# Performance work log

Measured on AMD Instinct MI355X. Metric: run time of the kernel, lower is better.

The kernel has to match this reference:

```python
import jax, jax.numpy as jnp
import numpy as np

D = 256; HEADS = 8; POINTS = 4; LAYERS = 6; HGT = 100; WID = 100; DH = D // HEADS


def _ln(x, g, b, eps=1e-5):
    m = x.mean(-1, keepdims=True)
    v = ((x - m) ** 2).mean(-1, keepdims=True)
    return (x - m) * jax.lax.rsqrt(v + eps) * g + b


def _bilinear(img, locs):
    # img: [B, H, W, C]; locs: [B, N, 2] normalized (x, y) in [0,1]
    # matches F.grid_sample(align_corners=False, padding_mode='zeros')
    B, H, W, C = img.shape
    flat = img.reshape(B, H * W, C)
    x = locs[..., 0] * W - 0.5
    y = locs[..., 1] * H - 0.5
    x0 = jnp.floor(x).astype(jnp.int32); y0 = jnp.floor(y).astype(jnp.int32)
    wx1 = x - x0; wx0 = 1.0 - wx1
    wy1 = y - y0; wy0 = 1.0 - wy1

    def corner(xi, yi, wgt):
        valid = (xi >= 0) & (xi < W) & (yi >= 0) & (yi < H)
        idx = jnp.clip(yi, 0, H - 1) * W + jnp.clip(xi, 0, W - 1)
        v = jnp.take_along_axis(flat, idx[..., None], axis=1)  # [B,N,C]
        return v * (wgt * valid)[..., None]

    return (corner(x0, y0, wx0 * wy0) + corner(x0 + 1, y0, wx1 * wy0)
            + corner(x0, y0 + 1, wx0 * wy1) + corner(x0 + 1, y0 + 1, wx1 * wy1))


def _forward(features, pos_embed, level_embed, off_w, off_b, aw_w, aw_b,
             val_w, val_b, out_w, out_b, ln1_g, ln1_b,
             ffn_w1, ffn_b1, ffn_w2, ffn_b2, ln3_g, ln3_b):
    bs, c, h, w = features.shape
    S = h * w
    src = features.reshape(bs, c, S).transpose(0, 2, 1)  # [bs,S,D]
    pos = pos_embed.reshape(bs, c, S).transpose(0, 2, 1) + level_embed[None, None, :]
    # reference points: pixel centers normalized; valid_ratios == 1 (no padding)
    ry = (jnp.arange(h, dtype=src.dtype) + 0.5) / h
    rx = (jnp.arange(w, dtype=src.dtype) + 0.5) / w
    ref = jnp.stack(jnp.meshgrid(rx, ry, indexing='xy'), -1).reshape(S, 2)  # [S,2] (x,y)
    norm = jnp.array([w, h], dtype=src.dtype)
    for l in range(LAYERS):
        q = src + pos  # with_pos_embed
        value = (src @ val_w[l] + val_b[l]).reshape(bs, S, HEADS, DH)
        off = (q @ off_w[l] + off_b[l]).reshape(bs, S, HEADS, POINTS, 2)
        attw = jax.nn.softmax((q @ aw_w[l] + aw_b[l]).reshape(bs, S, HEADS, POINTS), axis=-1)
        loc = ref[None, :, None, None, :] + off / norm  # [bs,S,H,P,2]
        img = value.transpose(0, 2, 1, 3).reshape(bs * HEADS, h, w, DH)
        locs = loc.transpose(0, 2, 1, 3, 4).reshape(bs * HEADS, S * POINTS, 2)
        samp = _bilinear(img, locs).reshape(bs, HEADS, S, POINTS, DH)
        attn = jnp.einsum('bhspd,bshp->bshd', samp, attw).reshape(bs, S, D)
        attn = attn @ out_w[l] + out_b[l]
        src = _ln(src + attn, ln1_g[l], ln1_b[l])  # norm1_xy (unit_dim*2 == d_model)
        ff = jax.nn.relu(src @ ffn_w1[l] + ffn_b1[l]) @ ffn_w2[l] + ffn_b2[l]
        src = _ln(src + ff, ln3_g[l], ln3_b[l])
    return src


def setup_inputs() -> dict:
    key = jax.random.key(0)
    ks = jax.random.split(key, 12)
    bs = 2
    s = 0.02
    rnd = lambda k, shape: jax.random.normal(k, shape, jnp.float32) * s
    return {
        'features': jax.random.normal(ks[0], (bs, D, HGT, WID), jnp.float32),
        'pos_embed': jax.random.normal(ks[1], (bs, D, HGT, WID), jnp.float32),
        'level_embed': rnd(ks[2], (D,)),
        'off_w': rnd(ks[3], (LAYERS, D, HEADS * POINTS * 2)),
        'off_b': rnd(ks[4], (LAYERS, HEADS * POINTS * 2)),
        'aw_w': rnd(ks[5], (LAYERS, D, HEADS * POINTS)),
        'aw_b': jnp.zeros((LAYERS, HEADS * POINTS), jnp.float32),
        'val_w': rnd(ks[6], (LAYERS, D, D)),
        'val_b': jnp.zeros((LAYERS, D), jnp.float32),
        'out_w': rnd(ks[7], (LAYERS, D, D)),
        'out_b': jnp.zeros((LAYERS, D), jnp.float32),
        'ln1_g': jnp.ones((LAYERS, D), jnp.float32),
        'ln1_b': jnp.zeros((LAYERS, D), jnp.float32),
        'ffn_w1': rnd(ks[8], (LAYERS, D, D)),
        'ffn_b1': jnp.zeros((LAYERS, D), jnp.float32),
        'ffn_w2': rnd(ks[9], (LAYERS, D, D)),
        'ffn_b2': jnp.zeros((LAYERS, D), jnp.float32),
        'ln3_g': jnp.ones((LAYERS, D), jnp.float32),
        'ln3_b': jnp.zeros((LAYERS, D), jnp.float32),
    }


def reference(features, pos_embed, level_embed, off_w, off_b, aw_w, aw_b,
              val_w, val_b, out_w, out_b, ln1_g, ln1_b,
              ffn_w1, ffn_b1, ffn_w2, ffn_b2, ln3_g, ln3_b):
    return _forward(features, pos_embed, level_embed, off_w, off_b, aw_w, aw_b,
                    val_w, val_b, out_w, out_b, ln1_g, ln1_b,
                    ffn_w1, ffn_b1, ffn_w2, ffn_b2, ln3_g, ln3_b)
```

## Files before the change

### kernel.cpp

```cpp
#include <hip/hip_runtime.h>
#include <math.h>

#define HGT 100
#define WID 100
#define S_TOK (HGT * WID)
#define D_MODEL 256
#define N_HEADS 8
#define DH 32
#define N_POINTS 4
#define N_LAYERS 6
#define BS 2
#define M_TOK (BS * S_TOK)

typedef __attribute__((ext_vector_type(8))) short short8v;
typedef __attribute__((ext_vector_type(4))) short short4v;
typedef __attribute__((ext_vector_type(4))) float f32x4;

__device__ __forceinline__ short f2bf(float f) {
  union { float f; unsigned u; } v; v.f = f;
  unsigned r = v.u + 0x7fff + ((v.u >> 16) & 1);
  return (short)(r >> 16);
}
__device__ __forceinline__ float bf2f(short s) {
  union { unsigned u; float f; } v;
  v.u = ((unsigned)(unsigned short)s) << 16;
  return v.f;
}

__global__ __launch_bounds__(256) void prep_tokens(
    const float* __restrict__ feat, const float* __restrict__ posin,
    const float* __restrict__ level, short* __restrict__ posb,
    short* __restrict__ srcb, short* __restrict__ qb) {
  __shared__ float tf[32][33];
  __shared__ float tp[32][33];
  int b = blockIdx.z;
  int s0 = blockIdx.x * 32;
  int c0 = blockIdx.y * 32;
  int tx = threadIdx.x, ty = threadIdx.y;
#pragma unroll
  for (int i = 0; i < 4; ++i) {
    int c = c0 + ty + i * 8;
    int s = s0 + tx;
    bool ok = s < S_TOK;
    size_t o = ((size_t)b * D_MODEL + c) * S_TOK + s;
    tf[ty + i * 8][tx] = ok ? feat[o] : 0.f;
    tp[ty + i * 8][tx] = ok ? posin[o] : 0.f;
  }
  __syncthreads();
#pragma unroll
  for (int i = 0; i < 4; ++i) {
    int s = s0 + ty + i * 8;
    int c = c0 + tx;
    if (s < S_TOK) {
      float f = tf[tx][ty + i * 8];
      float p = tp[tx][ty + i * 8] + level[c];
      size_t o = ((size_t)b * S_TOK + s) * D_MODEL + c;
      short pb = f2bf(p);
      posb[o] = pb;
      srcb[o] = f2bf(f);
      qb[o] = f2bf(f + bf2f(pb));
    }
  }
}

__global__ __launch_bounds__(256) void prep_weights(
    const float* __restrict__ val_w, const float* __restrict__ out_w,
    const float* __restrict__ ffn_w1, const float* __restrict__ ffn_w2,
    const float* __restrict__ off_w, const float* __restrict__ aw_w,
    short* __restrict__ wv, short* __restrict__ wo, short* __restrict__ w1t,
    short* __restrict__ w2t, short* __restrict__ woa) {
  int z = blockIdx.z;
  int l = z / 6, widx = z - (z / 6) * 6;
  const float* s;
  short* d;
  int N;
  if (widx == 0)      { s = val_w  + (size_t)l * 65536; d = wv  + (size_t)l * 65536; N = 256; }
  else if (widx == 1) { s = out_w  + (size_t)l * 65536; d = wo  + (size_t)l * 65536; N = 256; }
  else if (widx == 2) { s = ffn_w1 + (size_t)l * 65536; d = w1t + (size_t)l * 65536; N = 256; }
  else if (widx == 3) { s = ffn_w2 + (size_t)l * 65536; d = w2t + (size_t)l * 65536; N = 256; }
  else if (widx == 4) { s = off_w + (size_t)l * 256 * 64; d = woa + (size_t)l * 96 * 256; N = 64; }
  else                { s = aw_w  + (size_t)l * 256 * 32; d = woa + (size_t)l * 96 * 256 + (size_t)64 * 256; N = 32; }
  int n0 = blockIdx.x * 32, k0 = blockIdx.y * 32;
  if (n0 >= N) return;
  __shared__ float t[32][33];
  int tx = threadIdx.x, ty = threadIdx.y;
#pragma unroll
  for (int i = 0; i < 4; ++i) {
    int k = k0 + ty + i * 8;
    int n = n0 + tx;
    t[ty + i * 8][tx] = (n < N) ? s[(size_t)k * N + n] : 0.f;
  }
  __syncthreads();
#pragma unroll
  for (int i = 0; i < 4; ++i) {
    int n = n0 + ty + i * 8;
    int k = k0 + tx;
    if (n < N) d[(size_t)n * 256 + k] = f2bf(t[tx][ty + i * 8]);
  }
}

__global__ void biascat_kernel(const float* __restrict__ ob,
                               const float* __restrict__ ab,
                               float* __restrict__ dst) {
  int l = blockIdx.x, i = threadIdx.x;
  dst[l * 96 + i] = (i < 64) ? ob[l * 64 + i] : ab[l * 32 + (i - 64)];
}

__global__ __launch_bounds__(512) void gemm_vq(
    const short* __restrict__ srcb, const short* __restrict__ qb,
    const short* __restrict__ WV, const short* __restrict__ WOA,
    const float* __restrict__ vb, const float* __restrict__ b96,
    short* __restrict__ value, float* __restrict__ offaw) {
  __shared__ short lds[(256 + 64) * 72];
  short* As = lds;
  short* Bs = lds + 64 * 72;
  int tid = threadIdx.x;
  int wave = tid >> 6, lane = tid & 63;
  int lr = lane & 15, kb = lane >> 4;
  int bx = blockIdx.x;

  if (bx < 313) {
    int wr = wave >> 2, wc = wave & 3;
    int bm = bx * 64;
    int arow = tid >> 3, ach = (tid & 7) * 8;
    int brow = tid >> 1, bch = (tid & 1) * 32;
    bool aok = (bm + arow) < M_TOK;
    const short* aptr = srcb + (size_t)(bm + arow) * 256 + ach;
    const short* bptr = WV + (size_t)brow * 256 + bch;
    short* asd = &As[arow * 72 + ach];
    short* bsd = &Bs[brow * 72 + bch];

    f32x4 acc[2][4] = {};
    for (int k0 = 0; k0 < 256; k0 += 64) {
      short8v a0 = {};
      if (aok) a0 = *reinterpret_cast<const short8v*>(aptr + k0);
      *reinterpret_cast<short8v*>(asd) = a0;
#pragma unroll
      for (int j = 0; j < 4; ++j)
        *reinterpret_cast<short8v*>(bsd + j * 8) =
            *reinterpret_cast<const short8v*>(bptr + k0 + j * 8);
      __syncthreads();
#pragma unroll
      for (int ks = 0; ks < 2; ++ks) {
        short8v af[2], bf[4];
#pragma unroll
        for (int i = 0; i < 2; ++i)
          af[i] = *reinterpret_cast<const short8v*>(
              &As[(wr * 32 + i * 16 + lr) * 72 + ks * 32 + kb * 8]);
#pragma unroll
        for (int j = 0; j < 4; ++j)
          bf[j] = *reinterpret_cast<const short8v*>(
              &Bs[(wc * 64 + j * 16 + lr) * 72 + ks * 32 + kb * 8]);
#pragma unroll
        for (int i = 0; i < 2; ++i)
#pragma unroll
          for (int j = 0; j < 4; ++j)
            acc[i][j] = __builtin_amdgcn_mfma_f32_16x16x32_bf16(
                af[i], bf[j], acc[i][j], 0, 0, 0);
      }
      __syncthreads();
    }
    float bb[4];
#pragma unroll
    for (int fn = 0; fn < 4; ++fn) bb[fn] = vb[wc * 64 + fn * 16 + lr];
#pragma unroll
    for (int fm = 0; fm < 2; ++fm)
#pragma unroll
      for (int i = 0; i < 4; ++i) {
        int r = bm + wr * 32 + fm * 16 + kb * 4 + i;
        if (r >= M_TOK) continue;
#pragma unroll
        for (int fn = 0; fn < 4; ++fn) {
          int c = wc * 64 + fn * 16 + lr;
          value[(size_t)r * 256 + c] = f2bf(acc[fm][fn][i] + bb[fn]);
        }
      }
  } else {
    int wr = wave >> 2, wc = wave & 3;
    int bm = (bx - 313) * 64;
    int arow = tid >> 3, ach = (tid & 7) * 8;
    int brow = tid >> 2, bch = (tid & 3) * 16;
    bool aok = (bm + arow) < M_TOK;
    bool bok = brow < 96;
    const short* aptr = qb + (size_t)(bm + arow) * 256 + ach;
    const short* bptr = WOA + (size_t)brow * 256 + bch;
    short* asd = &As[arow * 72 + ach];
    short* bsd = &Bs[brow * 72 + bch];

    f32x4 acc[2][2] = {};
    for (int k0 = 0; k0 < 256; k0 += 64) {
      short8v a0 = {};
      if (aok) a0 = *reinterpret_cast<const short8v*>(aptr + k0);
      *reinterpret_cast<short8v*>(asd) = a0;
      short8v b0 = {}, b1 = {};
      if (bok) {
        b0 = *reinterpret_cast<const short8v*>(bptr + k0);
        b1 = *reinterpret_cast<const short8v*>(bptr + k0 + 8);
      }
      *reinterpret_cast<short8v*>(bsd) = b0;
      *reinterpret_cast<short8v*>(bsd + 8) = b1;
      __syncthreads();
#pragma unroll
      for (int ks = 0; ks < 2; ++ks) {
        short8v af[2], bf[2];
#pragma unroll
        for (int i = 0; i < 2; ++i)
          af[i] = *reinterpret_cast<const short8v*>(
              &As[(wr * 32 + i * 16 + lr) * 72 + ks * 32 + kb * 8]);
#pragma unroll
        for (int j = 0; j < 2; ++j)
          bf[j] = *reinterpret_cast<const short8v*>(
              &Bs[(wc * 32 + j * 16 + lr) * 72 + ks * 32 + kb * 8]);
#pragma unroll
        for (int i = 0; i < 2; ++i)
#pragma unroll
          for (int j = 0; j < 2; ++j)
            acc[i][j] = __builtin_amdgcn_mfma_f32_16x16x32_bf16(
                af[i], bf[j], acc[i][j], 0, 0, 0);
      }
      __syncthreads();
    }
#pragma unroll
    for (int fn = 0; fn < 2; ++fn) {
      int c = wc * 32 + fn * 16 + lr;
      if (c >= 96) continue;
      float bv = b96[c];
#pragma unroll
      for (int fm = 0; fm < 2; ++fm)
#pragma unroll
        for (int i = 0; i < 4; ++i) {
          int r = bm + wr * 32 + fm * 16 + kb * 4 + i;
          if (r < M_TOK) offaw[(size_t)r * 96 + c] = acc[fm][fn][i] + bv;
        }
    }
  }
}

__global__ __launch_bounds__(512) void gemm_out_ln1(
    const short* __restrict__ A, const short* __restrict__ WT,
    const float* __restrict__ bias, short* __restrict__ resid,
    const float* __restrict__ g, const float* __restrict__ lnb) {
  __shared__ short As[64 * 72];
  __shared__ short Bs[256 * 72];
  int tid = threadIdx.x;
  int wave = tid >> 6, lane = tid & 63;
  int lr = lane & 15, kb = lane >> 4;
  int wr = wave >> 2, wc = wave & 3;
  int bm = blockIdx.x * 64;

  int arow = tid >> 3, ach = (tid & 7) * 8;
  int brow = tid >> 1, bch = (tid & 1) * 32;
  bool aok = (bm + arow) < M_TOK;
  const short* aptr = A + (size_t)(bm + arow) * 256 + ach;
  const short* bptr = WT + (size_t)brow * 256 + bch;
  short* asd = &As[arow * 72 + ach];
  short* bsd = &Bs[brow * 72 + bch];

  f32x4 acc[2][4] = {};

  for (int k0 = 0; k0 < 256; k0 += 64) {
    short8v a0 = {};
    if (aok) a0 = *reinterpret_cast<const short8v*>(aptr + k0);
    *reinterpret_cast<short8v*>(asd) = a0;
#pragma unroll
    for (int j = 0; j < 4; ++j)
      *reinterpret_cast<short8v*>(bsd + j * 8) =
          *reinterpret_cast<const short8v*>(bptr + k0 + j * 8);
    __syncthreads();
#pragma unroll
    for (int ks = 0; ks < 2; ++ks) {
      short8v af[2], bf[4];
#pragma unroll
      for (int i = 0; i < 2; ++i)
        af[i] = *reinterpret_cast<const short8v*>(
            &As[(wr * 32 + i * 16 + lr) * 72 + ks * 32 + kb * 8]);
#pragma unroll
      for (int j = 0; j < 4; ++j)
        bf[j] = *reinterpret_cast<const short8v*>(
            &Bs[(wc * 64 + j * 16 + lr) * 72 + ks * 32 + kb * 8]);
#pragma unroll
      for (int i = 0; i < 2; ++i)
#pragma unroll
        for (int j = 0; j < 4; ++j)
          acc[i][j] = __builtin_amdgcn_mfma_f32_16x16x32_bf16(af[i], bf[j],
                                                              acc[i][j], 0, 0, 0);
    }
    __syncthreads();
  }

  float bb[4];
#pragma unroll
  for (int fn = 0; fn < 4; ++fn) bb[fn] = bias[wc * 64 + fn * 16 + lr];

  float* lns = (float*)As;
  float* lnq = lns + 256;
  float mean_[2][4], rs_[2][4];
#pragma unroll
  for (int fm = 0; fm < 2; ++fm)
#pragma unroll
    for (int i = 0; i < 4; ++i) {
      int lrow = wr * 32 + fm * 16 + kb * 4 + i;
      int r = bm + lrow;
      bool ok = r < M_TOK;
      float s = 0.f, q = 0.f;
#pragma unroll
      for (int fn = 0; fn < 4; ++fn) {
        int c = wc * 64 + fn * 16 + lr;
        float v = acc[fm][fn][i] + bb[fn];
        if (ok) v += bf2f(resid[(size_t)r * 256 + c]);
        acc[fm][fn][i] = v;
        s += v; q += v * v;
      }
#pragma unroll
      for (int o = 1; o < 16; o <<= 1) {
        s += __shfl_xor(s, o);
        q += __shfl_xor(q, o);
      }
      if (lr == 0) { lns[lrow * 4 + wc] = s; lnq[lrow * 4 + wc] = q; }
    }
  __syncthreads();
#pragma unroll
  for (int fm = 0; fm < 2; ++fm)
#pragma unroll
    for (int i = 0; i < 4; ++i) {
      int lrow = wr * 32 + fm * 16 + kb * 4 + i;
      float S = lns[lrow * 4 + 0] + lns[lrow * 4 + 1] + lns[lrow * 4 + 2] +
                lns[lrow * 4 + 3];
      float Q = lnq[lrow * 4 + 0] + lnq[lrow * 4 + 1] + lnq[lrow * 4 + 2] +
                lnq[lrow * 4 + 3];
      float mean = S * (1.f / 256.f);
      float var = Q * (1.f / 256.f) - mean * mean;
      mean_[fm][i] = mean;
      rs_[fm][i] = rsqrtf(var + 1e-5f);
    }
  float g4[4], lb4[4];
#pragma unroll
  for (int fn = 0; fn < 4; ++fn) {
    int c = wc * 64 + fn * 16 + lr;
    g4[fn] = g[c]; lb4[fn] = lnb[c];
  }
#pragma unroll
  for (int fm = 0; fm < 2; ++fm)
#pragma unroll
    for (int i = 0; i < 4; ++i) {
      int r = bm + wr * 32 + fm * 16 + kb * 4 + i;
      if (r >= M_TOK) continue;
#pragma unroll
      for (int fn = 0; fn < 4; ++fn) {
        int c = wc * 64 + fn * 16 + lr;
        float o = (acc[fm][fn][i] - mean_[fm][i]) * rs_[fm][i] * g4[fn] + lb4[fn];
        resid[(size_t)r * 256 + c] = f2bf(o);
      }
    }
}

template <int MODE>
__global__ __launch_bounds__(512) void gemm_ffn_ln3(
    const short* __restrict__ A, const short* __restrict__ W1T,
    const float* __restrict__ b1, const short* __restrict__ W2T,
    const float* __restrict__ b2, short* __restrict__ resid,
    float* __restrict__ outf, short* __restrict__ qb,
    const short* __restrict__ posb, const float* __restrict__ g,
    const float* __restrict__ lnb) {
  __shared__ short As[64 * 72];
  __shared__ short Bs[256 * 72];
  __shared__ short Hs[64 * 264];
  int tid = threadIdx.x;
  int wave = tid >> 6, lane = tid & 63;
  int lr = lane & 15, kb = lane >> 4;
  int wr = wave >> 2, wc = wave & 3;
  int bm = blockIdx.x * 64;

  int arow = tid >> 3, ach = (tid & 7) * 8;
  int brow = tid >> 1, bch = (tid & 1) * 32;
  bool aok = (bm + arow) < M_TOK;
  const short* aptr = A + (size_t)(bm + arow) * 256 + ach;
  short* asd = &As[arow * 72 + ach];
  short* bsd = &Bs[brow * 72 + bch];

  f32x4 acc[2][4] = {};

  {
    const short* bptr = W1T + (size_t)brow * 256 + bch;
    for (int k0 = 0; k0 < 256; k0 += 64) {
      short8v a0 = {};
      if (aok) a0 = *reinterpret_cast<const short8v*>(aptr + k0);
      *reinterpret_cast<short8v*>(asd) = a0;
#pragma unroll
      for (int j = 0; j < 4; ++j)
        *reinterpret_cast<short8v*>(bsd + j * 8) =
            *reinterpret_cast<const short8v*>(bptr + k0 + j * 8);
      __syncthreads();
#pragma unroll
      for (int ks = 0; ks < 2; ++ks) {
        short8v af[2], bf[4];
#pragma unroll
        for (int i = 0; i < 2; ++i)
          af[i] = *reinterpret_cast<const short8v*>(
              &As[(wr * 32 + i * 16 + lr) * 72 + ks * 32 + kb * 8]);
#pragma unroll
        for (int j = 0; j < 4; ++j)
          bf[j] = *reinterpret_cast<const short8v*>(
              &Bs[(wc * 64 + j * 16 + lr) * 72 + ks * 32 + kb * 8]);
#pragma unroll
        for (int i = 0; i < 2; ++i)
#pragma unroll
          for (int j = 0; j < 4; ++j)
            acc[i][j] = __builtin_amdgcn_mfma_f32_16x16x32_bf16(
                af[i], bf[j], acc[i][j], 0, 0, 0);
      }
      __syncthreads();
    }
    float bb1[4];
#pragma unroll
    for (int fn = 0; fn < 4; ++fn) bb1[fn] = b1[wc * 64 + fn * 16 + lr];
#pragma unroll
    for (int fm = 0; fm < 2; ++fm)
#pragma unroll
      for (int i = 0; i < 4; ++i) {
        int lrow = wr * 32 + fm * 16 + kb * 4 + i;
#pragma unroll
        for (int fn = 0; fn < 4; ++fn) {
          int c = wc * 64 + fn * 16 + lr;
          float v = fmaxf(acc[fm][fn][i] + bb1[fn], 0.f);
          Hs[lrow * 264 + c] = f2bf(v);
        }
      }
  }

#pragma unroll
  for (int fm = 0; fm < 2; ++fm)
#pragma unroll
    for (int fn = 0; fn < 4; ++fn) acc[fm][fn] = f32x4{0.f, 0.f, 0.f, 0.f};
  {
    const short* bptr = W2T + (size_t)brow * 256 + bch;
    for (int k0 = 0; k0 < 256; k0 += 64) {
#pragma unroll
      for (int j = 0; j < 4; ++j)
        *reinterpret_cast<short8v*>(bsd + j * 8) =
            *reinterpret_cast<const short8v*>(bptr + k0 + j * 8);
      __syncthreads();
#pragma unroll
      for (int ks = 0; ks < 2; ++ks) {
        short8v af[2], bf[4];
#pragma unroll
        for (int i = 0; i < 2; ++i)
          af[i] = *reinterpret_cast<const short8v*>(
              &Hs[(wr * 32 + i * 16 + lr) * 264 + k0 + ks * 32 + kb * 8]);
#pragma unroll
        for (int j = 0; j < 4; ++j)
          bf[j] = *reinterpret_cast<const short8v*>(
              &Bs[(wc * 64 + j * 16 + lr) * 72 + ks * 32 + kb * 8]);
#pragma unroll
        for (int i = 0; i < 2; ++i)
#pragma unroll
          for (int j = 0; j < 4; ++j)
            acc[i][j] = __builtin_amdgcn_mfma_f32_16x16x32_bf16(
                af[i], bf[j], acc[i][j], 0, 0, 0);
      }
      __syncthreads();
    }
  }

  float bb[4];
#pragma unroll
  for (int fn = 0; fn < 4; ++fn) bb[fn] = b2[wc * 64 + fn * 16 + lr];

  float* lns = (float*)As;
  float* lnq = lns + 256;
  float mean_[2][4], rs_[2][4];
#pragma unroll
  for (int fm = 0; fm < 2; ++fm)
#pragma unroll
    for (int i = 0; i < 4; ++i) {
      int lrow = wr * 32 + fm * 16 + kb * 4 + i;
      int r = bm + lrow;
      bool ok = r < M_TOK;
      float s = 0.f, q = 0.f;
#pragma unroll
      for (int fn = 0; fn < 4; ++fn) {
        int c = wc * 64 + fn * 16 + lr;
        float v = acc[fm][fn][i] + bb[fn];
        if (ok) v += bf2f(resid[(size_t)r * 256 + c]);
        acc[fm][fn][i] = v;
        s += v; q += v * v;
      }
#pragma unroll
      for (int o = 1; o < 16; o <<= 1) {
        s += __shfl_xor(s, o);
        q += __shfl_xor(q, o);
      }
      if (lr == 0) { lns[lrow * 4 + wc] = s; lnq[lrow * 4 + wc] = q; }
    }
  __syncthreads();
#pragma unroll
  for (int fm = 0; fm < 2; ++fm)
#pragma unroll
    for (int i = 0; i < 4; ++i) {
      int lrow = wr * 32 + fm * 16 + kb * 4 + i;
      float S = lns[lrow * 4 + 0] + lns[lrow * 4 + 1] + lns[lrow * 4 + 2] +
                lns[lrow * 4 + 3];
      float Q = lnq[lrow * 4 + 0] + lnq[lrow * 4 + 1] + lnq[lrow * 4 + 2] +
                lnq[lrow * 4 + 3];
      float mean = S * (1.f / 256.f);
      float var = Q * (1.f / 256.f) - mean * mean;
      mean_[fm][i] = mean;
      rs_[fm][i] = rsqrtf(var + 1e-5f);
    }
  float g4[4], lb4[4];
#pragma unroll
  for (int fn = 0; fn < 4; ++fn) {
    int c = wc * 64 + fn * 16 + lr;
    g4[fn] = g[c]; lb4[fn] = lnb[c];
  }
#pragma unroll
  for (int fm = 0; fm < 2; ++fm)
#pragma unroll
    for (int i = 0; i < 4; ++i) {
      int r = bm + wr * 32 + fm * 16 + kb * 4 + i;
      if (r >= M_TOK) continue;
#pragma unroll
      for (int fn = 0; fn < 4; ++fn) {
        int c = wc * 64 + fn * 16 + lr;
        float o = (acc[fm][fn][i] - mean_[fm][i]) * rs_[fm][i] * g4[fn] + lb4[fn];
        if (MODE == 3) {
          outf[(size_t)r * 256 + c] = o;
        } else {
          resid[(size_t)r * 256 + c] = f2bf(o);
          qb[(size_t)r * 256 + c] = f2bf(o + bf2f(posb[(size_t)r * 256 + c]));
        }
      }
    }
}

__global__ __launch_bounds__(256) void sample_kernel(
    const short* __restrict__ value, const float* __restrict__ offaw,
    short* __restrict__ attn) {
  __shared__ float loff[8][64];
  __shared__ float lw[8][32];
  int bid = blockIdx.x;
  int xcd = bid & 7, idx = bid >> 3;
  int swz = (xcd < 4 ? xcd * 313 : 4 * 313 + (xcd - 4) * 312) + idx;
  int tok0 = swz * 8;
  int tid = threadIdx.x;
  for (int i = tid; i < 768; i += 256) {
    int t = i / 96, j = i - t * 96;
    float v = offaw[(size_t)(tok0 + t) * 96 + j];
    if (j < 64) loff[t][j] = v; else lw[t][j - 64] = v;
  }
  __syncthreads();
  if (tid < 64) {
    int t = tid >> 3, h = tid & 7;
    float* w = &lw[t][h * 4];
    float m = fmaxf(fmaxf(w[0], w[1]), fmaxf(w[2], w[3]));
    float e0 = __expf(w[0] - m), e1 = __expf(w[1] - m);
    float e2 = __expf(w[2] - m), e3 = __expf(w[3] - m);
    float inv = 1.f / (e0 + e1 + e2 + e3);
    w[0] = e0 * inv; w[1] = e1 * inv; w[2] = e2 * inv; w[3] = e3 * inv;
  }
  __syncthreads();

  int ts = tid >> 5, lane = tid & 31;
  int token = tok0 + ts;
  int h = lane >> 2, d8 = (lane & 3) * 8;
  int b = token / S_TOK;
  int s = token - b * S_TOK;
  int ix = s % WID, iy = s / WID;
  const short* vbase = value + ((size_t)b * S_TOK) * D_MODEL + h * DH + d8;

  float acc[8] = {};
#pragma unroll
  for (int p = 0; p < N_POINTS; ++p) {
    float ox = loff[ts][h * 8 + p * 2 + 0];
    float oy = loff[ts][h * 8 + p * 2 + 1];
    float aw = lw[ts][h * 4 + p];
    float px = (float)ix + ox;
    float py = (float)iy + oy;
    float x0f = floorf(px), y0f = floorf(py);
    int x0 = (int)x0f, y0 = (int)y0f;
    float wx1 = px - x0f, wx0 = 1.f - wx1;
    float wy1 = py - y0f, wy0 = 1.f - wy1;
    float sv[8] = {};
    bool xa = (x0 >= 0) & (x0 < WID), xb = (x0 + 1 >= 0) & (x0 + 1 < WID);
    bool ya = (y0 >= 0) & (y0 < HGT), yb = (y0 + 1 >= 0) & (y0 + 1 < HGT);
#define CORNER(XOK, YOK, XI, YI, WGT)                                        \
    if ((XOK) & (YOK)) {                                                     \
      short8v v = *reinterpret_cast<const short8v*>(                         \
          vbase + (size_t)((YI) * WID + (XI)) * D_MODEL);                    \
      float wg = (WGT);                                                      \
      _Pragma("unroll")                                                      \
      for (int j = 0; j < 8; ++j) sv[j] = fmaf(wg, bf2f(v[j]), sv[j]);       \
    }
    CORNER(xa, ya, x0, y0, wx0 * wy0)
    CORNER(xb, ya, x0 + 1, y0, wx1 * wy0)
    CORNER(xa, yb, x0, y0 + 1, wx0 * wy1)
    CORNER(xb, yb, x0 + 1, y0 + 1, wx1 * wy1)
#undef CORNER
#pragma unroll
    for (int j = 0; j < 8; ++j) acc[j] = fmaf(aw, sv[j], acc[j]);
  }
  short8v o;
#pragma unroll
  for (int j = 0; j < 8; ++j) o[j] = f2bf(acc[j]);
  *reinterpret_cast<short8v*>(attn + (size_t)token * D_MODEL + h * DH + d8) = o;
}

extern "C" void kernel_launch(void* const* d_in, const int* in_sizes, int n_in,
                              void* d_out, int out_size, void* d_ws,
                              size_t ws_size, hipStream_t stream) {
  const float* features  = (const float*)d_in[0];
  const float* pos_embed = (const float*)d_in[1];
  const float* level_emb = (const float*)d_in[2];
  const float* off_w = (const float*)d_in[3];
  const float* off_b = (const float*)d_in[4];
  const float* aw_w  = (const float*)d_in[5];
  const float* aw_b  = (const float*)d_in[6];
  const float* val_w = (const float*)d_in[7];
  const float* val_b = (const float*)d_in[8];
  const float* out_w = (const float*)d_in[9];
  const float* out_b = (const float*)d_in[10];
  const float* ln1_g = (const float*)d_in[11];
  const float* ln1_b = (const float*)d_in[12];
  const float* ffn_w1 = (const float*)d_in[13];
  const float* ffn_b1 = (const float*)d_in[14];
  const float* ffn_w2 = (const float*)d_in[15];
  const float* ffn_b2 = (const float*)d_in[16];
  const float* ln3_g = (const float*)d_in[17];
  const float* ln3_b = (const float*)d_in[18];

  float* ws = (float*)d_ws;
  const size_t BIG = (size_t)M_TOK * D_MODEL;
  float* offaw = ws;
  short* posb  = (short*)(offaw + (size_t)M_TOK * 96);
  short* srcb  = posb + BIG;
  short* qb    = srcb + BIG;
  short* value = qb + BIG;
  short* attn  = value + BIG;
  short* wv  = attn + BIG;
  short* wo  = wv + (size_t)6 * 65536;
  short* w1t = wo + (size_t)6 * 65536;
  short* w2t = w1t + (size_t)6 * 65536;
  short* woa = w2t + (size_t)6 * 65536;
  float* bias96 = (float*)(woa + (size_t)6 * 96 * 256);

  prep_tokens<<<dim3(313, 8, 2), dim3(32, 8), 0, stream>>>(
      features, pos_embed, level_emb, posb, srcb, qb);
  prep_weights<<<dim3(8, 8, 36), dim3(32, 8), 0, stream>>>(
      val_w, out_w, ffn_w1, ffn_w2, off_w, aw_w, wv, wo, w1t, w2t, woa);
  biascat_kernel<<<dim3(6), dim3(96), 0, stream>>>(off_b, aw_b, bias96);

  for (int l = 0; l < N_LAYERS; ++l) {
    const short* wvl = wv + (size_t)l * 65536;
    const short* wol = wo + (size_t)l * 65536;
    const short* w1l = w1t + (size_t)l * 65536;
    const short* w2l = w2t + (size_t)l * 65536;
    const short* woal = woa + (size_t)l * 96 * 256;

    gemm_vq<<<626, 512, 0, stream>>>(srcb, qb, wvl, woal,
                                     val_b + (size_t)l * 256,
                                     bias96 + (size_t)l * 96, value, offaw);
    sample_kernel<<<M_TOK / 8, 256, 0, stream>>>(value, offaw, attn);
    gemm_out_ln1<<<313, 512, 0, stream>>>(
        attn, wol, out_b + (size_t)l * 256, srcb,
        ln1_g + (size_t)l * 256, ln1_b + (size_t)l * 256);
    if (l == N_LAYERS - 1) {
      gemm_ffn_ln3<3><<<313, 512, 0, stream>>>(
          srcb, w1l, ffn_b1 + (size_t)l * 256, w2l, ffn_b2 + (size_t)l * 256,
          srcb, (float*)d_out, nullptr, nullptr,
          ln3_g + (size_t)l * 256, ln3_b + (size_t)l * 256);
    } else {
      gemm_ffn_ln3<2><<<313, 512, 0, stream>>>(
          srcb, w1l, ffn_b1 + (size_t)l * 256, w2l, ffn_b2 + (size_t)l * 256,
          srcb, nullptr, qb, posb,
          ln3_g + (size_t)l * 256, ln3_b + (size_t)l * 256);
    }
  }
}
```

Before: 490.5 us.

## Fuse deformable bilinear sampling into output-projection GEMM with LN1

Removes the separate sampling kernel and its attn buffer. The out-projection GEMM now first computes softmax and bilinear sampling per token-head into shared memory (full 64x256 A tile), then runs the MFMA GEMM and LayerNorm. This eliminates a global write and read of the attention output and one launch per layer, but each thread now handles a whole head (32 channels) with many registers. Only 313 blocks do the gather, which reduces parallelism for the memory-latency-bound sampling.

```diff
diff --git a/kernel.cpp b/kernel.cpp
--- a/kernel.cpp
+++ b/kernel.cpp
@@ -236,32 +236,100 @@
   }
 }
 
-__global__ __launch_bounds__(512) void gemm_out_ln1(
-    const short* __restrict__ A, const short* __restrict__ WT,
-    const float* __restrict__ bias, short* __restrict__ resid,
-    const float* __restrict__ g, const float* __restrict__ lnb) {
-  __shared__ short As[64 * 72];
+__global__ __launch_bounds__(512) void gemm_attn_ln1(
+    const short* __restrict__ value, const float* __restrict__ offaw,
+    const short* __restrict__ WT, const float* __restrict__ bias,
+    short* __restrict__ resid, const float* __restrict__ g,
+    const float* __restrict__ lnb) {
+  __shared__ short As[4 * 64 * 72];
   __shared__ short Bs[256 * 72];
   int tid = threadIdx.x;
   int wave = tid >> 6, lane = tid & 63;
   int lr = lane & 15, kb = lane >> 4;
   int wr = wave >> 2, wc = wave & 3;
-  int bm = blockIdx.x * 64;
-
-  int arow = tid >> 3, ach = (tid & 7) * 8;
+  int bid = blockIdx.x;
+  int xcd = bid & 7, idx = bid >> 3;
+  int swz = (xcd < 1 ? xcd * 40 : 40 + (xcd - 1) * 39) + idx;
+  int bm = swz * 64;
+
+  {
+    int lrow = tid >> 3;
+    int token = bm + lrow;
+    int h = tid & 7;
+    short* dst = &As[(h >> 1) * 4608 + lrow * 72 + (h & 1) * 32];
+    if (token < M_TOK) {
+      int b = token / S_TOK;
+      int s = token - b * S_TOK;
+      int ix = s % WID, iy = s / WID;
+      const float* oa = offaw + (size_t)token * 96;
+      float w4[4];
+      {
+        float l0 = oa[64 + h * 4 + 0], l1 = oa[64 + h * 4 + 1];
+        float l2 = oa[64 + h * 4 + 2], l3 = oa[64 + h * 4 + 3];
+        float m = fmaxf(fmaxf(l0, l1), fmaxf(l2, l3));
+        float e0 = __expf(l0 - m), e1 = __expf(l1 - m);
+        float e2 = __expf(l2 - m), e3 = __expf(l3 - m);
+        float inv = 1.f / (e0 + e1 + e2 + e3);
+        w4[0] = e0 * inv; w4[1] = e1 * inv; w4[2] = e2 * inv; w4[3] = e3 * inv;
+      }
+      const short* vbase = value + ((size_t)b * S_TOK) * 256 + h * 32;
+      float acc32[32] = {};
+#pragma unroll
+      for (int p = 0; p < 4; ++p) {
+        float ox = oa[h * 8 + p * 2 + 0];
+        float oy = oa[h * 8 + p * 2 + 1];
+        float aw = w4[p];
+        float px = (float)ix + ox;
+        float py = (float)iy + oy;
+        float x0f = floorf(px), y0f = floorf(py);
+        int x0 = (int)x0f, y0 = (int)y0f;
+        float wx1 = px - x0f, wx0 = 1.f - wx1;
+        float wy1 = py - y0f, wy0 = 1.f - wy1;
+        float sv[32] = {};
+        bool xa = (x0 >= 0) & (x0 < WID), xb = (x0 + 1 >= 0) & (x0 + 1 < WID);
+        bool ya = (y0 >= 0) & (y0 < HGT), yb = (y0 + 1 >= 0) & (y0 + 1 < HGT);
+#define CORNER32(XOK, YOK, XI, YI, WGT)                                      \
+        if ((XOK) & (YOK)) {                                                 \
+          const short* vp = vbase + (size_t)((YI) * WID + (XI)) * 256;       \
+          float wg = (WGT);                                                  \
+          _Pragma("unroll")                                                  \
+          for (int c8 = 0; c8 < 4; ++c8) {                                   \
+            short8v v = *reinterpret_cast<const short8v*>(vp + c8 * 8);      \
+            _Pragma("unroll")                                                \
+            for (int j = 0; j < 8; ++j)                                      \
+              sv[c8 * 8 + j] = fmaf(wg, bf2f(v[j]), sv[c8 * 8 + j]);         \
+          }                                                                  \
+        }
+        CORNER32(xa, ya, x0, y0, wx0 * wy0)
+        CORNER32(xb, ya, x0 + 1, y0, wx1 * wy0)
+        CORNER32(xa, yb, x0, y0 + 1, wx0 * wy1)
+        CORNER32(xb, yb, x0 + 1, y0 + 1, wx1 * wy1)
+#undef CORNER32
+#pragma unroll
+        for (int j = 0; j < 32; ++j) acc32[j] = fmaf(aw, sv[j], acc32[j]);
+      }
+#pragma unroll
+      for (int c8 = 0; c8 < 4; ++c8) {
+        short8v o;
+#pragma unroll
+        for (int j = 0; j < 8; ++j) o[j] = f2bf(acc32[c8 * 8 + j]);
+        *reinterpret_cast<short8v*>(dst + c8 * 8) = o;
+      }
+    } else {
+      short8v z = {};
+#pragma unroll
+      for (int c8 = 0; c8 < 4; ++c8)
+        *reinterpret_cast<short8v*>(dst + c8 * 8) = z;
+    }
+  }
+
   int brow = tid >> 1, bch = (tid & 1) * 32;
-  bool aok = (bm + arow) < M_TOK;
-  const short* aptr = A + (size_t)(bm + arow) * 256 + ach;
   const short* bptr = WT + (size_t)brow * 256 + bch;
-  short* asd = &As[arow * 72 + ach];
   short* bsd = &Bs[brow * 72 + bch];
 
   f32x4 acc[2][4] = {};
 
   for (int k0 = 0; k0 < 256; k0 += 64) {
-    short8v a0 = {};
-    if (aok) a0 = *reinterpret_cast<const short8v*>(aptr + k0);
-    *reinterpret_cast<short8v*>(asd) = a0;
 #pragma unroll
     for (int j = 0; j < 4; ++j)
       *reinterpret_cast<short8v*>(bsd + j * 8) =
@@ -273,7 +341,8 @@
 #pragma unroll
       for (int i = 0; i < 2; ++i)
         af[i] = *reinterpret_cast<const short8v*>(
-            &As[(wr * 32 + i * 16 + lr) * 72 + ks * 32 + kb * 8]);
+            &As[(k0 >> 6) * 4608 + (wr * 32 + i * 16 + lr) * 72 +
+                ks * 32 + kb * 8]);
 #pragma unroll
       for (int j = 0; j < 4; ++j)
         bf[j] = *reinterpret_cast<const short8v*>(
@@ -531,78 +600,6 @@
         }
       }
     }
-}
-
-__global__ __launch_bounds__(256) void sample_kernel(
-    const short* __restrict__ value, const float* __restrict__ offaw,
-    short* __restrict__ attn) {
-  __shared__ float loff[8][64];
-  __shared__ float lw[8][32];
-  int bid = blockIdx.x;
-  int xcd = bid & 7, idx = bid >> 3;
-  int swz = (xcd < 4 ? xcd * 313 : 4 * 313 + (xcd - 4) * 312) + idx;
-  int tok0 = swz * 8;
-  int tid = threadIdx.x;
-  for (int i = tid; i < 768; i += 256) {
-    int t = i / 96, j = i - t * 96;
-    float v = offaw[(size_t)(tok0 + t) * 96 + j];
-    if (j < 64) loff[t][j] = v; else lw[t][j - 64] = v;
-  }
-  __syncthreads();
-  if (tid < 64) {
-    int t = tid >> 3, h = tid & 7;
-    float* w = &lw[t][h * 4];
-    float m = fmaxf(fmaxf(w[0], w[1]), fmaxf(w[2], w[3]));
-    float e0 = __expf(w[0] - m), e1 = __expf(w[1] - m);
-    float e2 = __expf(w[2] - m), e3 = __expf(w[3] - m);
-    float inv = 1.f / (e0 + e1 + e2 + e3);
-    w[0] = e0 * inv; w[1] = e1 * inv; w[2] = e2 * inv; w[3] = e3 * inv;
-  }
-  __syncthreads();
-
-  int ts = tid >> 5, lane = tid & 31;
-  int token = tok0 + ts;
-  int h = lane >> 2, d8 = (lane & 3) * 8;
-  int b = token / S_TOK;
-  int s = token - b * S_TOK;
-  int ix = s % WID, iy = s / WID;
-  const short* vbase = value + ((size_t)b * S_TOK) * D_MODEL + h * DH + d8;
-
-  float acc[8] = {};
-#pragma unroll
-  for (int p = 0; p < N_POINTS; ++p) {
-    float ox = loff[ts][h * 8 + p * 2 + 0];
-    float oy = loff[ts][h * 8 + p * 2 + 1];
-    float aw = lw[ts][h * 4 + p];
-    float px = (float)ix + ox;
-    float py = (float)iy + oy;
-    float x0f = floorf(px), y0f = floorf(py);
-    int x0 = (int)x0f, y0 = (int)y0f;
-    float wx1 = px - x0f, wx0 = 1.f - wx1;
-    float wy1 = py - y0f, wy0 = 1.f - wy1;
-    float sv[8] = {};
-    bool xa = (x0 >= 0) & (x0 < WID), xb = (x0 + 1 >= 0) & (x0 + 1 < WID);
-    bool ya = (y0 >= 0) & (y0 < HGT), yb = (y0 + 1 >= 0) & (y0 + 1 < HGT);
-#define CORNER(XOK, YOK, XI, YI, WGT)                                        \
-    if ((XOK) & (YOK)) {                                                     \
-      short8v v = *reinterpret_cast<const short8v*>(                         \
-          vbase + (size_t)((YI) * WID + (XI)) * D_MODEL);                    \
-      float wg = (WGT);                                                      \
-      _Pragma("unroll")                                                      \
-      for (int j = 0; j < 8; ++j) sv[j] = fmaf(wg, bf2f(v[j]), sv[j]);       \
-    }
-    CORNER(xa, ya, x0, y0, wx0 * wy0)
-    CORNER(xb, ya, x0 + 1, y0, wx1 * wy0)
-    CORNER(xa, yb, x0, y0 + 1, wx0 * wy1)
-    CORNER(xb, yb, x0 + 1, y0 + 1, wx1 * wy1)
-#undef CORNER
-#pragma unroll
-    for (int j = 0; j < 8; ++j) acc[j] = fmaf(aw, sv[j], acc[j]);
-  }
-  short8v o;
-#pragma unroll
-  for (int j = 0; j < 8; ++j) o[j] = f2bf(acc[j]);
-  *reinterpret_cast<short8v*>(attn + (size_t)token * D_MODEL + h * DH + d8) = o;
 }
 
 extern "C" void kernel_launch(void* const* d_in, const int* in_sizes, int n_in,
@@ -635,8 +632,7 @@
   short* srcb  = posb + BIG;
   short* qb    = srcb + BIG;
   short* value = qb + BIG;
-  short* attn  = value + BIG;
-  short* wv  = attn + BIG;
+  short* wv  = value + BIG;
   short* wo  = wv + (size_t)6 * 65536;
   short* w1t = wo + (size_t)6 * 65536;
   short* w2t = w1t + (size_t)6 * 65536;
@@ -659,9 +655,8 @@
     gemm_vq<<<626, 512, 0, stream>>>(srcb, qb, wvl, woal,
                                      val_b + (size_t)l * 256,
                                      bias96 + (size_t)l * 96, value, offaw);
-    sample_kernel<<<M_TOK / 8, 256, 0, stream>>>(value, offaw, attn);
-    gemm_out_ln1<<<313, 512, 0, stream>>>(
-        attn, wol, out_b + (size_t)l * 256, srcb,
+    gemm_attn_ln1<<<313, 512, 0, stream>>>(
+        value, offaw, wol, out_b + (size_t)l * 256, srcb,
         ln1_g + (size_t)l * 256, ln1_b + (size_t)l * 256);
     if (l == N_LAYERS - 1) {
       gemm_ffn_ln3<3><<<313, 512, 0, stream>>>(
```

Result: slower. 596.5 us (+21.6%).

## Load GEMM tiles via direct global-to-LDS loads with XOR-swizzled layout

Applied to the files above, without the earlier changes.

Replaces the register-staged global-to-shared copies in all GEMM kernels with global_load_lds 16-byte direct loads into unpadded 64-wide LDS tiles. Bank conflicts are avoided with an XOR swizzle that is applied on the activation-load side and baked into the transposed weight layout during weight prep. The intent is to cut VGPR traffic, instruction count and LDS footprint from padding. The combined offset/attention-weight matrix is padded to 128 rows per layer so out-of-range rows can be loaded without bounds checks, and tail token rows are clamped instead of zeroed.

```diff
diff --git a/kernel.cpp b/kernel.cpp
--- a/kernel.cpp
+++ b/kernel.cpp
@@ -25,6 +25,12 @@
   union { unsigned u; float f; } v;
   v.u = ((unsigned)(unsigned short)s) << 16;
   return v.f;
+}
+
+__device__ __forceinline__ void gld16(const short* g, short* l) {
+  __builtin_amdgcn_global_load_lds(
+      (const __attribute__((address_space(1))) unsigned int*)g,
+      (__attribute__((address_space(3))) unsigned int*)l, 16, 0, 0);
 }
 
 __global__ __launch_bounds__(256) void prep_tokens(
@@ -78,8 +84,8 @@
   else if (widx == 1) { s = out_w  + (size_t)l * 65536; d = wo  + (size_t)l * 65536; N = 256; }
   else if (widx == 2) { s = ffn_w1 + (size_t)l * 65536; d = w1t + (size_t)l * 65536; N = 256; }
   else if (widx == 3) { s = ffn_w2 + (size_t)l * 65536; d = w2t + (size_t)l * 65536; N = 256; }
-  else if (widx == 4) { s = off_w + (size_t)l * 256 * 64; d = woa + (size_t)l * 96 * 256; N = 64; }
-  else                { s = aw_w  + (size_t)l * 256 * 32; d = woa + (size_t)l * 96 * 256 + (size_t)64 * 256; N = 32; }
+  else if (widx == 4) { s = off_w + (size_t)l * 256 * 64; d = woa + (size_t)l * 32768; N = 64; }
+  else                { s = aw_w  + (size_t)l * 256 * 32; d = woa + (size_t)l * 32768 + (size_t)64 * 256; N = 32; }
   int n0 = blockIdx.x * 32, k0 = blockIdx.y * 32;
   if (n0 >= N) return;
   __shared__ float t[32][33];
@@ -95,7 +101,11 @@
   for (int i = 0; i < 4; ++i) {
     int n = n0 + ty + i * 8;
     int k = k0 + tx;
-    if (n < N) d[(size_t)n * 256 + k] = f2bf(t[tx][ty + i * 8]);
+    if (n < N) {
+      int slot = ((k >> 3) & 7) ^ (n & 7);
+      size_t dk = (size_t)(k & ~63) + (slot << 3) + (k & 7);
+      d[(size_t)n * 256 + dk] = f2bf(t[tx][ty + i * 8]);
+    }
   }
 }
 
@@ -111,46 +121,46 @@
     const short* __restrict__ WV, const short* __restrict__ WOA,
     const float* __restrict__ vb, const float* __restrict__ b96,
     short* __restrict__ value, float* __restrict__ offaw) {
-  __shared__ short lds[(256 + 64) * 72];
-  short* As = lds;
-  short* Bs = lds + 64 * 72;
+  __shared__ __align__(16) short As[64 * 64];
+  __shared__ __align__(16) short Bs[256 * 64];
   int tid = threadIdx.x;
   int wave = tid >> 6, lane = tid & 63;
   int lr = lane & 15, kb = lane >> 4;
   int bx = blockIdx.x;
+  int sc16 = (lane & 7) ^ ((lane >> 3) & 7);
+  int r7 = lr & 7;
+  int sl0 = (kb ^ r7) << 3;
+  int sl1 = ((4 + kb) ^ r7) << 3;
 
   if (bx < 313) {
     int wr = wave >> 2, wc = wave & 3;
     int bm = bx * 64;
-    int arow = tid >> 3, ach = (tid & 7) * 8;
-    int brow = tid >> 1, bch = (tid & 1) * 32;
-    bool aok = (bm + arow) < M_TOK;
-    const short* aptr = srcb + (size_t)(bm + arow) * 256 + ach;
-    const short* bptr = WV + (size_t)brow * 256 + bch;
-    short* asd = &As[arow * 72 + ach];
-    short* bsd = &Bs[brow * 72 + bch];
+    int arow = bm + wave * 8 + (lane >> 3);
+    if (arow >= M_TOK) arow = M_TOK - 1;
+    const short* aS = srcb + (size_t)arow * 256 + sc16 * 8;
+    short* aD = As + wave * 512;
+    const short* bS = WV + (size_t)(wave * 32 + (lane >> 3)) * 256 + (lane & 7) * 8;
+    short* bD = Bs + wave * 32 * 64;
 
     f32x4 acc[2][4] = {};
     for (int k0 = 0; k0 < 256; k0 += 64) {
-      short8v a0 = {};
-      if (aok) a0 = *reinterpret_cast<const short8v*>(aptr + k0);
-      *reinterpret_cast<short8v*>(asd) = a0;
-#pragma unroll
-      for (int j = 0; j < 4; ++j)
-        *reinterpret_cast<short8v*>(bsd + j * 8) =
-            *reinterpret_cast<const short8v*>(bptr + k0 + j * 8);
+      gld16(aS + k0, aD);
+#pragma unroll
+      for (int c = 0; c < 4; ++c)
+        gld16(bS + (size_t)(c * 8) * 256 + k0, bD + c * 8 * 64);
       __syncthreads();
 #pragma unroll
       for (int ks = 0; ks < 2; ++ks) {
+        int sl = ks ? sl1 : sl0;
         short8v af[2], bf[4];
 #pragma unroll
         for (int i = 0; i < 2; ++i)
           af[i] = *reinterpret_cast<const short8v*>(
-              &As[(wr * 32 + i * 16 + lr) * 72 + ks * 32 + kb * 8]);
+              &As[(wr * 32 + i * 16 + lr) * 64 + sl]);
 #pragma unroll
         for (int j = 0; j < 4; ++j)
           bf[j] = *reinterpret_cast<const short8v*>(
-              &Bs[(wc * 64 + j * 16 + lr) * 72 + ks * 32 + kb * 8]);
+              &Bs[(wc * 64 + j * 16 + lr) * 64 + sl]);
 #pragma unroll
         for (int i = 0; i < 2; ++i)
 #pragma unroll
@@ -178,39 +188,32 @@
   } else {
     int wr = wave >> 2, wc = wave & 3;
     int bm = (bx - 313) * 64;
-    int arow = tid >> 3, ach = (tid & 7) * 8;
-    int brow = tid >> 2, bch = (tid & 3) * 16;
-    bool aok = (bm + arow) < M_TOK;
-    bool bok = brow < 96;
-    const short* aptr = qb + (size_t)(bm + arow) * 256 + ach;
-    const short* bptr = WOA + (size_t)brow * 256 + bch;
-    short* asd = &As[arow * 72 + ach];
-    short* bsd = &Bs[brow * 72 + bch];
+    int arow = bm + wave * 8 + (lane >> 3);
+    if (arow >= M_TOK) arow = M_TOK - 1;
+    const short* aS = qb + (size_t)arow * 256 + sc16 * 8;
+    short* aD = As + wave * 512;
+    const short* bS = WOA + (size_t)(wave * 16 + (lane >> 3)) * 256 + (lane & 7) * 8;
+    short* bD = Bs + wave * 16 * 64;
 
     f32x4 acc[2][2] = {};
     for (int k0 = 0; k0 < 256; k0 += 64) {
-      short8v a0 = {};
-      if (aok) a0 = *reinterpret_cast<const short8v*>(aptr + k0);
-      *reinterpret_cast<short8v*>(asd) = a0;
-      short8v b0 = {}, b1 = {};
-      if (bok) {
-        b0 = *reinterpret_cast<const short8v*>(bptr + k0);
-        b1 = *reinterpret_cast<const short8v*>(bptr + k0 + 8);
-      }
-      *reinterpret_cast<short8v*>(bsd) = b0;
-      *reinterpret_cast<short8v*>(bsd + 8) = b1;
+      gld16(aS + k0, aD);
+#pragma unroll
+      for (int c = 0; c < 2; ++c)
+        gld16(bS + (size_t)(c * 8) * 256 + k0, bD + c * 8 * 64);
       __syncthreads();
 #pragma unroll
       for (int ks = 0; ks < 2; ++ks) {
+        int sl = ks ? sl1 : sl0;
         short8v af[2], bf[2];
 #pragma unroll
         for (int i = 0; i < 2; ++i)
           af[i] = *reinterpret_cast<const short8v*>(
-              &As[(wr * 32 + i * 16 + lr) * 72 + ks * 32 + kb * 8]);
+              &As[(wr * 32 + i * 16 + lr) * 64 + sl]);
 #pragma unroll
         for (int j = 0; j < 2; ++j)
           bf[j] = *reinterpret_cast<const short8v*>(
-              &Bs[(wc * 32 + j * 16 + lr) * 72 + ks * 32 + kb * 8]);
+              &Bs[(wc * 32 + j * 16 + lr) * 64 + sl]);
 #pragma unroll
         for (int i = 0; i < 2; ++i)
 #pragma unroll
@@ -240,44 +243,45 @@
     const short* __restrict__ A, const short* __restrict__ WT,
     const float* __restrict__ bias, short* __restrict__ resid,
     const float* __restrict__ g, const float* __restrict__ lnb) {
-  __shared__ short As[64 * 72];
-  __shared__ short Bs[256 * 72];
+  __shared__ __align__(16) short As[64 * 64];
+  __shared__ __align__(16) short Bs[256 * 64];
   int tid = threadIdx.x;
   int wave = tid >> 6, lane = tid & 63;
   int lr = lane & 15, kb = lane >> 4;
   int wr = wave >> 2, wc = wave & 3;
   int bm = blockIdx.x * 64;
-
-  int arow = tid >> 3, ach = (tid & 7) * 8;
-  int brow = tid >> 1, bch = (tid & 1) * 32;
-  bool aok = (bm + arow) < M_TOK;
-  const short* aptr = A + (size_t)(bm + arow) * 256 + ach;
-  const short* bptr = WT + (size_t)brow * 256 + bch;
-  short* asd = &As[arow * 72 + ach];
-  short* bsd = &Bs[brow * 72 + bch];
+  int sc16 = (lane & 7) ^ ((lane >> 3) & 7);
+  int r7 = lr & 7;
+  int sl0 = (kb ^ r7) << 3;
+  int sl1 = ((4 + kb) ^ r7) << 3;
+
+  int arow = bm + wave * 8 + (lane >> 3);
+  if (arow >= M_TOK) arow = M_TOK - 1;
+  const short* aS = A + (size_t)arow * 256 + sc16 * 8;
+  short* aD = As + wave * 512;
+  const short* bS = WT + (size_t)(wave * 32 + (lane >> 3)) * 256 + (lane & 7) * 8;
+  short* bD = Bs + wave * 32 * 64;
 
   f32x4 acc[2][4] = {};
 
   for (int k0 = 0; k0 < 256; k0 += 64) {
-    short8v a0 = {};
-    if (aok) a0 = *reinterpret_cast<const short8v*>(aptr + k0);
-    *reinterpret_cast<short8v*>(asd) = a0;
-#pragma unroll
-    for (int j = 0; j < 4; ++j)
-      *reinterpret_cast<short8v*>(bsd + j * 8) =
-          *reinterpret_cast<const short8v*>(bptr + k0 + j * 8);
+    gld16(aS + k0, aD);
+#pragma unroll
+    for (int c = 0; c < 4; ++c)
+      gld16(bS + (size_t)(c * 8) * 256 + k0, bD + c * 8 * 64);
     __syncthreads();
 #pragma unroll
     for (int ks = 0; ks < 2; ++ks) {
+      int sl = ks ? sl1 : sl0;
       short8v af[2], bf[4];
 #pragma unroll
       for (int i = 0; i < 2; ++i)
         af[i] = *reinterpret_cast<const short8v*>(
-            &As[(wr * 32 + i * 16 + lr) * 72 + ks * 32 + kb * 8]);
+            &As[(wr * 32 + i * 16 + lr) * 64 + sl]);
 #pragma unroll
       for (int j = 0; j < 4; ++j)
         bf[j] = *reinterpret_cast<const short8v*>(
-            &Bs[(wc * 64 + j * 16 + lr) * 72 + ks * 32 + kb * 8]);
+            &Bs[(wc * 64 + j * 16 + lr) * 64 + sl]);
 #pragma unroll
       for (int i = 0; i < 2; ++i)
 #pragma unroll
@@ -362,46 +366,49 @@
     float* __restrict__ outf, short* __restrict__ qb,
     const short* __restrict__ posb, const float* __restrict__ g,
     const float* __restrict__ lnb) {
-  __shared__ short As[64 * 72];
-  __shared__ short Bs[256 * 72];
-  __shared__ short Hs[64 * 264];
+  __shared__ __align__(16) short As[64 * 64];
+  __shared__ __align__(16) short Bs[256 * 64];
+  __shared__ __align__(16) short Hs[64 * 264];
   int tid = threadIdx.x;
   int wave = tid >> 6, lane = tid & 63;
   int lr = lane & 15, kb = lane >> 4;
   int wr = wave >> 2, wc = wave & 3;
   int bm = blockIdx.x * 64;
-
-  int arow = tid >> 3, ach = (tid & 7) * 8;
-  int brow = tid >> 1, bch = (tid & 1) * 32;
-  bool aok = (bm + arow) < M_TOK;
-  const short* aptr = A + (size_t)(bm + arow) * 256 + ach;
-  short* asd = &As[arow * 72 + ach];
-  short* bsd = &Bs[brow * 72 + bch];
+  int sc16 = (lane & 7) ^ ((lane >> 3) & 7);
+  int r7 = lr & 7;
+  int sl0 = (kb ^ r7) << 3;
+  int sl1 = ((4 + kb) ^ r7) << 3;
+
+  int arow = bm + wave * 8 + (lane >> 3);
+  if (arow >= M_TOK) arow = M_TOK - 1;
+  const short* aS = A + (size_t)arow * 256 + sc16 * 8;
+  short* aD = As + wave * 512;
+  short* bD = Bs + wave * 32 * 64;
+  int brow0 = wave * 32 + (lane >> 3);
+  int bcol = (lane & 7) * 8;
 
   f32x4 acc[2][4] = {};
 
   {
-    const short* bptr = W1T + (size_t)brow * 256 + bch;
+    const short* bS = W1T + (size_t)brow0 * 256 + bcol;
     for (int k0 = 0; k0 < 256; k0 += 64) {
-      short8v a0 = {};
-      if (aok) a0 = *reinterpret_cast<const short8v*>(aptr + k0);
-      *reinterpret_cast<short8v*>(asd) = a0;
-#pragma unroll
-      for (int j = 0; j < 4; ++j)
-        *reinterpret_cast<short8v*>(bsd + j * 8) =
-            *reinterpret_cast<const short8v*>(bptr + k0 + j * 8);
+      gld16(aS + k0, aD);
+#pragma unroll
+      for (int c = 0; c < 4; ++c)
+        gld16(bS + (size_t)(c * 8) * 256 + k0, bD + c * 8 * 64);
       __syncthreads();
 #pragma unroll
       for (int ks = 0; ks < 2; ++ks) {
+        int sl = ks ? sl1 : sl0;
         short8v af[2], bf[4];
 #pragma unroll
         for (int i = 0; i < 2; ++i)
           af[i] = *reinterpret_cast<const short8v*>(
-              &As[(wr * 32 + i * 16 + lr) * 72 + ks * 32 + kb * 8]);
+              &As[(wr * 32 + i * 16 + lr) * 64 + sl]);
 #pragma unroll
         for (int j = 0; j < 4; ++j)
           bf[j] = *reinterpret_cast<const short8v*>(
-              &Bs[(wc * 64 + j * 16 + lr) * 72 + ks * 32 + kb * 8]);
+              &Bs[(wc * 64 + j * 16 + lr) * 64 + sl]);
 #pragma unroll
         for (int i = 0; i < 2; ++i)
 #pragma unroll
@@ -433,15 +440,15 @@
 #pragma unroll
     for (int fn = 0; fn < 4; ++fn) acc[fm][fn] = f32x4{0.f, 0.f, 0.f, 0.f};
   {
-    const short* bptr = W2T + (size_t)brow * 256 + bch;
+    const short* bS = W2T + (size_t)brow0 * 256 + bcol;
     for (int k0 = 0; k0 < 256; k0 += 64) {
 #pragma unroll
-      for (int j = 0; j < 4; ++j)
-        *reinterpret_cast<short8v*>(bsd + j * 8) =
-            *reinterpret_cast<const short8v*>(bptr + k0 + j * 8);
+      for (int c = 0; c < 4; ++c)
+        gld16(bS + (size_t)(c * 8) * 256 + k0, bD + c * 8 * 64);
       __syncthreads();
 #pragma unroll
       for (int ks = 0; ks < 2; ++ks) {
+        int sl = ks ? sl1 : sl0;
         short8v af[2], bf[4];
 #pragma unroll
         for (int i = 0; i < 2; ++i)
@@ -450,7 +457,7 @@
 #pragma unroll
         for (int j = 0; j < 4; ++j)
           bf[j] = *reinterpret_cast<const short8v*>(
-              &Bs[(wc * 64 + j * 16 + lr) * 72 + ks * 32 + kb * 8]);
+              &Bs[(wc * 64 + j * 16 + lr) * 64 + sl]);
 #pragma unroll
         for (int i = 0; i < 2; ++i)
 #pragma unroll
@@ -641,7 +648,7 @@
   short* w1t = wo + (size_t)6 * 65536;
   short* w2t = w1t + (size_t)6 * 65536;
   short* woa = w2t + (size_t)6 * 65536;
-  float* bias96 = (float*)(woa + (size_t)6 * 96 * 256);
+  float* bias96 = (float*)(woa + (size_t)6 * 32768);
 
   prep_tokens<<<dim3(313, 8, 2), dim3(32, 8), 0, stream>>>(
       features, pos_embed, level_emb, posb, srcb, qb);
@@ -654,7 +661,7 @@
     const short* wol = wo + (size_t)l * 65536;
     const short* w1l = w1t + (size_t)l * 65536;
     const short* w2l = w2t + (size_t)l * 65536;
-    const short* woal = woa + (size_t)l * 96 * 256;
+    const short* woal = woa + (size_t)l * 32768;
 
     gemm_vq<<<626, 512, 0, stream>>>(srcb, qb, wvl, woal,
                                      val_b + (size_t)l * 256,
```

Result: faster. 441.3 us, median of 2 (-10.0%).
